# Performance work log

Measured on AMD Instinct MI355X. Metric: run time of the kernel, lower is better.

Reference implementation:

```python
import jax, jax.numpy as jnp
import numpy as np

WS = 7
NHEAD = 8


def setup_inputs() -> dict:
    key = jax.random.key(0)
    k1, k2, k3 = jax.random.split(key, 3)
    B, H, W, D = 32, 56, 56, 256
    x = jax.random.normal(k1, (B, H, W, D), dtype=jnp.float32)
    in_proj_w = jax.random.normal(k2, (3 * D, D), dtype=jnp.float32) * 0.02
    in_proj_b = jnp.zeros((3 * D,), dtype=jnp.float32)
    out_w = jax.random.normal(k3, (D, D), dtype=jnp.float32) * 0.02
    out_b = jnp.zeros((D,), dtype=jnp.float32)
    return {"x": x, "in_proj_w": in_proj_w, "in_proj_b": in_proj_b,
            "out_w": out_w, "out_b": out_b}


def reference(x, in_proj_w, in_proj_b, out_w, out_b):
    B, Hf, Wf, D = x.shape
    ws = WS
    hd = D // NHEAD
    pad_h = (-Hf) % ws
    pad_w = (-Wf) % ws
    xp = jnp.pad(x, ((0, 0), (0, pad_h), (0, pad_w), (0, 0)))
    Hp, Wp = Hf + pad_h, Wf + pad_w
    nh, nw = Hp // ws, Wp // ws
    # partition into windows: [B*nh*nw, ws*ws, D]
    xw = xp.reshape(B, nh, ws, nw, ws, D).transpose(0, 1, 3, 2, 4, 5)
    xw = xw.reshape(B * nh * nw, ws * ws, D)
    N, L = xw.shape[0], ws * ws
    # qkv projection (torch MHA: x @ in_proj_w.T + in_proj_b)
    qkv = jnp.einsum('nld,ed->nle', xw, in_proj_w) + in_proj_b  # [N, L, 3D]
    q, k, v = jnp.split(qkv, 3, axis=-1)
    q = q.reshape(N, L, NHEAD, hd).transpose(0, 2, 1, 3)
    k = k.reshape(N, L, NHEAD, hd).transpose(0, 2, 1, 3)
    v = v.reshape(N, L, NHEAD, hd).transpose(0, 2, 1, 3)
    scale = 1.0 / np.sqrt(hd).astype(np.float32)
    scores = jnp.einsum('nhqd,nhkd->nhqk', q * scale, k)  # [N, H, L, L]
    attn = jax.nn.softmax(scores, axis=-1)
    o = jnp.einsum('nhqk,nhkd->nhqd', attn, v)
    o = o.transpose(0, 2, 1, 3).reshape(N, L, D)
    o = jnp.einsum('nld,ed->nle', o, out_w) + out_b
    # un-window
    o = o.reshape(B, nh, nw, ws, ws, D).transpose(0, 1, 3, 2, 4, 5)
    o = o.reshape(B, Hp, Wp, D)
    return o[:, :Hf, :Wf, :]
```

## Files before the change

### kernel.cpp

```cpp
#include <hip/hip_runtime.h>


using f16   = _Float16;
using f16x4 = __attribute__((ext_vector_type(4))) _Float16;
using f16x8 = __attribute__((ext_vector_type(8))) _Float16;
using f32x4 = __attribute__((ext_vector_type(4))) float;

#define NTOK   100352
#define DMODEL 256
#define QKVN   768

typedef const __attribute__((address_space(1))) unsigned int* as1_u32p;
typedef __attribute__((address_space(3))) unsigned int* as3_u32p;

__device__ __forceinline__ void gload16(const void* g, void* l) {
    __builtin_amdgcn_global_load_lds((as1_u32p)g, (as3_u32p)l, 16, 0, 0);
}

__device__ __forceinline__ f16x8 zero8() {
    f16x8 z;
#pragma unroll
    for (int i = 0; i < 8; ++i) z[i] = (f16)0;
    return z;
}

#define XV4   6422528
#define WQV4  49152
__global__ __launch_bounds__(256) void convert_all(
    const float* __restrict__ X, const float* __restrict__ Wq,
    f16* __restrict__ Xh, f16* __restrict__ Wqh)
{
    const float scale = 0.17677669529663687f;
    const int total = XV4 + WQV4;
    for (int i = blockIdx.x * blockDim.x + threadIdx.x; i < total;
         i += gridDim.x * blockDim.x) {
        float4 f;
        f16x4 h;
        if (i < XV4) {
            f = reinterpret_cast<const float4*>(X)[i];
            h[0]=(f16)f.x; h[1]=(f16)f.y; h[2]=(f16)f.z; h[3]=(f16)f.w;
            reinterpret_cast<f16x4*>(Xh)[i] = h;
        } else {
            int idx = i - XV4;
            int row = idx >> 6;
            float sc = (row < 256) ? scale : 1.0f;
            f = reinterpret_cast<const float4*>(Wq)[idx];
            h[0]=(f16)(f.x*sc); h[1]=(f16)(f.y*sc); h[2]=(f16)(f.z*sc); h[3]=(f16)(f.w*sc);
            reinterpret_cast<f16x4*>(Wqh)[idx] = h;
        }
    }
}

__global__ __launch_bounds__(256) void qkv_gemm(
    const f16* __restrict__ Xh,
    const f16* __restrict__ Wh,
    const float* __restrict__ bias,
    f16* __restrict__ QKV)
{
    __shared__ f16 As[128 * 64];
    __shared__ f16 Bs[128 * 64];
    const int tid  = threadIdx.x;
    const int lane = tid & 63;
    const int wave = tid >> 6;
    int wg = blockIdx.x;
    const int cpx = (NTOK / 128) * (QKVN / 128) / 8;
    wg = (wg & 7) * cpx + (wg >> 3);
    const int m0 = (wg / (QKVN / 128)) * 128;
    const int n0 = (wg % (QKVN / 128)) * 128;
    const int wm = (wave >> 1) * 64;
    const int wn = (wave & 1) * 64;
    const int g  = lane >> 4;
    const int lr = lane & 15;

    f32x4 acc[4][4] = {};

    for (int k0 = 0; k0 < 256; k0 += 64) {
#pragma unroll
        for (int j = 0; j < 4; ++j) {
            int s   = wave * 64 + lane + j * 256;
            int row = s >> 3;
            int cs  = (s & 7) ^ (row & 7);
            gload16(Xh + (size_t)(m0 + row) * 256 + k0 + cs * 8,
                    &As[(size_t)(wave * 64 + j * 256) * 8]);
            gload16(Wh + (size_t)(n0 + row) * 256 + k0 + cs * 8,
                    &Bs[(size_t)(wave * 64 + j * 256) * 8]);
        }
        __syncthreads();
#pragma unroll
        for (int ks = 0; ks < 2; ++ks) {
            f16x8 a[4], b[4];
#pragma unroll
            for (int i = 0; i < 4; ++i) {
                int row = wm + i * 16 + lr;
                int c   = ((ks << 2) + g) ^ (row & 7);
                a[i] = *reinterpret_cast<const f16x8*>(&As[row * 64 + c * 8]);
            }
#pragma unroll
            for (int i = 0; i < 4; ++i) {
                int row = wn + i * 16 + lr;
                int c   = ((ks << 2) + g) ^ (row & 7);
                b[i] = *reinterpret_cast<const f16x8*>(&Bs[row * 64 + c * 8]);
            }
#pragma unroll
            for (int mi = 0; mi < 4; ++mi)
#pragma unroll
                for (int ni = 0; ni < 4; ++ni)
                    acc[mi][ni] = __builtin_amdgcn_mfma_f32_16x16x32_f16(a[mi], b[ni], acc[mi][ni], 0, 0, 0);
        }
        __syncthreads();
    }
    const float scale = 0.17677669529663687f;
#pragma unroll
    for (int ni = 0; ni < 4; ++ni) {
        int n = n0 + wn + ni * 16 + lr;
        float bv = bias[n];
        if (n < 256) bv *= scale;
#pragma unroll
        for (int mi = 0; mi < 4; ++mi)
#pragma unroll
            for (int r = 0; r < 4; ++r) {
                int m = m0 + wm + mi * 16 + g * 4 + r;
                QKV[(size_t)m * QKVN + n] = (f16)(acc[mi][ni][r] + bv);
            }
    }
}

__global__ __launch_bounds__(256) void win_attn(f16* __restrict__ QKV)
{
    __shared__ f16 Vt[4][32][68];
    __shared__ f16 P[4][64][68];
    const int tid  = threadIdx.x;
    const int lane = tid & 63;
    const int w    = tid >> 6;
    const int u    = blockIdx.x * 4 + w;
    const int win = u >> 3, h = u & 7;
    const int b = win >> 6, wh = (win >> 3) & 7, ww = win & 7;
    const int base = (b * 56 + wh * 7) * 56 + ww * 7;
    const int g = lane >> 4, lr = lane & 15;

    auto tok = [&](int row) { int rr = row / 7; return base + rr * 56 + (row - rr * 7); };

    f16x8 qf[4], kf[4];
#pragma unroll
    for (int i = 0; i < 4; ++i) {
        int row = i * 16 + lr;
        if (row < 49) {
            size_t off = (size_t)tok(row) * QKVN + h * 32 + g * 8;
            qf[i] = *reinterpret_cast<const f16x8*>(QKV + off);
            kf[i] = *reinterpret_cast<const f16x8*>(QKV + off + 256);
        } else { qf[i] = zero8(); kf[i] = zero8(); }
    }
    {
        int kk = lane;
        if (kk < 49) {
            size_t off = (size_t)tok(kk) * QKVN + 512 + h * 32;
            f16x8 vv[4];
#pragma unroll
            for (int j = 0; j < 4; ++j)
                vv[j] = *reinterpret_cast<const f16x8*>(QKV + off + j * 8);
#pragma unroll
            for (int j = 0; j < 4; ++j)
#pragma unroll
                for (int d = 0; d < 8; ++d) Vt[w][j * 8 + d][kk] = vv[j][d];
        } else {
#pragma unroll
            for (int d = 0; d < 32; ++d) Vt[w][d][kk] = (f16)0;
        }
    }
    f32x4 s[4][4] = {};
#pragma unroll
    for (int ki = 0; ki < 4; ++ki)
#pragma unroll
        for (int qi = 0; qi < 4; ++qi)
            s[ki][qi] = __builtin_amdgcn_mfma_f32_16x16x32_f16(kf[ki], qf[qi], s[ki][qi], 0, 0, 0);

#pragma unroll
    for (int qi = 0; qi < 4; ++qi) {
        float e[4][4];
        float sum = 0.f;
#pragma unroll
        for (int ki = 0; ki < 4; ++ki)
#pragma unroll
            for (int r = 0; r < 4; ++r)
                e[ki][r] = __expf(s[ki][qi][r]);
#pragma unroll
        for (int ki = 0; ki < 3; ++ki)
#pragma unroll
            for (int r = 0; r < 4; ++r)
                sum += e[ki][r];
        sum += (g == 0) ? e[3][0] : 0.f;
        sum += __shfl_xor(sum, 16, 64);
        sum += __shfl_xor(sum, 32, 64);
        float is = 1.f / sum;
#pragma unroll
        for (int ki = 0; ki < 4; ++ki) {
            f16x4 pw;
            pw[0] = (f16)(e[ki][0] * is);
            pw[1] = (f16)(e[ki][1] * is);
            pw[2] = (f16)(e[ki][2] * is);
            pw[3] = (f16)(e[ki][3] * is);
            *reinterpret_cast<f16x4*>(&P[w][qi * 16 + lr][ki * 16 + g * 4]) = pw;
        }
    }
    __syncthreads();

    f32x4 o[4][2] = {};
#pragma unroll
    for (int ks = 0; ks < 2; ++ks) {
        f16x8 pa[4], vb[2];
#pragma unroll
        for (int mi = 0; mi < 4; ++mi)
            pa[mi] = *reinterpret_cast<const f16x8*>(&P[w][mi * 16 + lr][ks * 32 + g * 8]);
#pragma unroll
        for (int ni = 0; ni < 2; ++ni)
            vb[ni] = *reinterpret_cast<const f16x8*>(&Vt[w][ni * 16 + lr][ks * 32 + g * 8]);
#pragma unroll
        for (int mi = 0; mi < 4; ++mi)
#pragma unroll
            for (int ni = 0; ni < 2; ++ni)
                o[mi][ni] = __builtin_amdgcn_mfma_f32_16x16x32_f16(pa[mi], vb[ni], o[mi][ni], 0, 0, 0);
    }
#pragma unroll
    for (int mi = 0; mi < 4; ++mi)
#pragma unroll
        for (int r = 0; r < 4; ++r) {
            int row = mi * 16 + g * 4 + r;
            if (row < 49) {
                size_t off = (size_t)tok(row) * QKVN + h * 32;
#pragma unroll
                for (int ni = 0; ni < 2; ++ni)
                    QKV[off + ni * 16 + lr] = (f16)o[mi][ni][r];
            }
        }
}

__global__ __launch_bounds__(256) void out_gemm(
    const f16* __restrict__ O,
    const float* __restrict__ W,
    const float* __restrict__ bias,
    float* __restrict__ OUT)
{
    __shared__ f16 As[128 * 64];
    __shared__ f16 Bs[128][72];
    const int tid  = threadIdx.x;
    const int lane = tid & 63;
    const int wave = tid >> 6;
    int wg = blockIdx.x;
    const int cpx = (NTOK / 128) * (DMODEL / 128) / 8;
    wg = (wg & 7) * cpx + (wg >> 3);
    const int m0 = (wg / (DMODEL / 128)) * 128;
    const int n0 = (wg % (DMODEL / 128)) * 128;
    const int wm = (wave >> 1) * 64;
    const int wn = (wave & 1) * 64;
    const int g  = lane >> 4;
    const int lr = lane & 15;

    f32x4 acc[4][4] = {};

    for (int k0 = 0; k0 < 256; k0 += 64) {
#pragma unroll
        for (int j = 0; j < 4; ++j) {
            int s   = wave * 64 + lane + j * 256;
            int row = s >> 3;
            int cs  = (s & 7) ^ (row & 7);
            gload16(O + (size_t)(m0 + row) * QKVN + k0 + cs * 8,
                    &As[(size_t)(wave * 64 + j * 256) * 8]);
        }
#pragma unroll
        for (int j = 0; j < 8; ++j) {
            int v = tid + j * 256;
            int row = v >> 4, cv = v & 15;
            float4 f = *reinterpret_cast<const float4*>(W + (size_t)(n0 + row) * 256 + k0 + cv * 4);
            f16x4 h; h[0]=(f16)f.x; h[1]=(f16)f.y; h[2]=(f16)f.z; h[3]=(f16)f.w;
            *reinterpret_cast<f16x4*>(&Bs[row][cv * 4]) = h;
        }
        __syncthreads();
#pragma unroll
        for (int ks = 0; ks < 2; ++ks) {
            f16x8 a[4], b[4];
#pragma unroll
            for (int i = 0; i < 4; ++i) {
                int row = wm + i * 16 + lr;
                int c   = ((ks << 2) + g) ^ (row & 7);
                a[i] = *reinterpret_cast<const f16x8*>(&As[row * 64 + c * 8]);
            }
#pragma unroll
            for (int i = 0; i < 4; ++i)
                b[i] = *reinterpret_cast<const f16x8*>(&Bs[wn + i * 16 + lr][ks * 32 + g * 8]);
#pragma unroll
            for (int mi = 0; mi < 4; ++mi)
#pragma unroll
                for (int ni = 0; ni < 4; ++ni)
                    acc[mi][ni] = __builtin_amdgcn_mfma_f32_16x16x32_f16(a[mi], b[ni], acc[mi][ni], 0, 0, 0);
        }
        __syncthreads();
    }
#pragma unroll
    for (int ni = 0; ni < 4; ++ni) {
        int n = n0 + wn + ni * 16 + lr;
        float bv = bias[n];
#pragma unroll
        for (int mi = 0; mi < 4; ++mi)
#pragma unroll
            for (int r = 0; r < 4; ++r) {
                int m = m0 + wm + mi * 16 + g * 4 + r;
                OUT[(size_t)m * 256 + n] = acc[mi][ni][r] + bv;
            }
    }
}

extern "C" void kernel_launch(void* const* d_in, const int* in_sizes, int n_in,
                              void* d_out, int out_size, void* d_ws, size_t ws_size,
                              hipStream_t stream) {
    const float* x     = (const float*)d_in[0];
    const float* in_w  = (const float*)d_in[1];
    const float* in_b  = (const float*)d_in[2];
    const float* out_w = (const float*)d_in[3];
    const float* out_b = (const float*)d_in[4];
    float* out = (float*)d_out;
    f16* qkv = (f16*)d_ws;

    f16* xh  = (f16*)d_out;
    f16* wqh = xh + (size_t)NTOK * 256;

    convert_all<<<2048, 256, 0, stream>>>(x, in_w, xh, wqh);

    qkv_gemm<<<(NTOK / 128) * (QKVN / 128), 256, 0, stream>>>(xh, wqh, in_b, qkv);

    win_attn<<<4096, 256, 0, stream>>>(qkv);

    out_gemm<<<(NTOK / 128) * (DMODEL / 128), 256, 0, stream>>>(qkv, out_w, out_b, out);
}
```

Before: 161.3 us.

## Double-buffer A tiles and keep full-K B tile resident in LDS for both GEMMs

Both projection GEMMs now use 512-thread blocks covering 256x128 output tiles. The full K=256 slice of the weight tile is loaded into LDS once up front, and the activation tile is double-buffered so the next K-step's load overlaps the current step's MFMAs. This targets the load-then-sync stalls and halves redundant weight traffic per output row. It raises LDS use to about 128KB per block, which limits occupancy to one block per CU.

```diff
diff --git a/kernel.cpp b/kernel.cpp
--- a/kernel.cpp
+++ b/kernel.cpp
@@ -51,41 +51,57 @@
     }
 }
 
-__global__ __launch_bounds__(256) void qkv_gemm(
+__global__ __launch_bounds__(512) void qkv_gemm(
     const f16* __restrict__ Xh,
     const f16* __restrict__ Wh,
     const float* __restrict__ bias,
     f16* __restrict__ QKV)
 {
-    __shared__ f16 As[128 * 64];
-    __shared__ f16 Bs[128 * 64];
+    __shared__ f16 As[2][256 * 64];
+    __shared__ f16 Bs[128 * 256];
     const int tid  = threadIdx.x;
     const int lane = tid & 63;
     const int wave = tid >> 6;
     int wg = blockIdx.x;
-    const int cpx = (NTOK / 128) * (QKVN / 128) / 8;
+    const int cpx = (NTOK / 256) * (QKVN / 128) / 8;
     wg = (wg & 7) * cpx + (wg >> 3);
-    const int m0 = (wg / (QKVN / 128)) * 128;
+    const int m0 = (wg / (QKVN / 128)) * 256;
     const int n0 = (wg % (QKVN / 128)) * 128;
     const int wm = (wave >> 1) * 64;
     const int wn = (wave & 1) * 64;
     const int g  = lane >> 4;
     const int lr = lane & 15;
 
+#pragma unroll
+    for (int j = 0; j < 8; ++j) {
+        int s   = tid + j * 512;
+        int row = s >> 5, sl = s & 31;
+        int ss  = sl ^ (row & 7);
+        gload16(Wh + (size_t)(n0 + row) * 256 + ss * 8, &Bs[s * 8]);
+    }
+#pragma unroll
+    for (int j = 0; j < 4; ++j) {
+        int s   = tid + j * 512;
+        int row = s >> 3, sl = s & 7;
+        int ss  = sl ^ (row & 7);
+        gload16(Xh + (size_t)(m0 + row) * 256 + ss * 8, &As[0][s * 8]);
+    }
+    __syncthreads();
+
     f32x4 acc[4][4] = {};
-
-    for (int k0 = 0; k0 < 256; k0 += 64) {
-#pragma unroll
-        for (int j = 0; j < 4; ++j) {
-            int s   = wave * 64 + lane + j * 256;
-            int row = s >> 3;
-            int cs  = (s & 7) ^ (row & 7);
-            gload16(Xh + (size_t)(m0 + row) * 256 + k0 + cs * 8,
-                    &As[(size_t)(wave * 64 + j * 256) * 8]);
-            gload16(Wh + (size_t)(n0 + row) * 256 + k0 + cs * 8,
-                    &Bs[(size_t)(wave * 64 + j * 256) * 8]);
-        }
-        __syncthreads();
+    int buf = 0;
+    for (int t = 0; t < 4; ++t) {
+        if (t < 3) {
+            int k0 = (t + 1) * 64;
+#pragma unroll
+            for (int j = 0; j < 4; ++j) {
+                int s   = tid + j * 512;
+                int row = s >> 3, sl = s & 7;
+                int ss  = sl ^ (row & 7);
+                gload16(Xh + (size_t)(m0 + row) * 256 + k0 + ss * 8,
+                        &As[buf ^ 1][s * 8]);
+            }
+        }
 #pragma unroll
         for (int ks = 0; ks < 2; ++ks) {
             f16x8 a[4], b[4];
@@ -93,13 +109,14 @@
             for (int i = 0; i < 4; ++i) {
                 int row = wm + i * 16 + lr;
                 int c   = ((ks << 2) + g) ^ (row & 7);
-                a[i] = *reinterpret_cast<const f16x8*>(&As[row * 64 + c * 8]);
+                a[i] = *reinterpret_cast<const f16x8*>(&As[buf][row * 64 + c * 8]);
             }
 #pragma unroll
             for (int i = 0; i < 4; ++i) {
                 int row = wn + i * 16 + lr;
-                int c   = ((ks << 2) + g) ^ (row & 7);
-                b[i] = *reinterpret_cast<const f16x8*>(&Bs[row * 64 + c * 8]);
+                int sl  = (t << 3) + (ks << 2) + g;
+                int c   = sl ^ (row & 7);
+                b[i] = *reinterpret_cast<const f16x8*>(&Bs[row * 256 + c * 8]);
             }
 #pragma unroll
             for (int mi = 0; mi < 4; ++mi)
@@ -108,6 +125,7 @@
                     acc[mi][ni] = __builtin_amdgcn_mfma_f32_16x16x32_f16(a[mi], b[ni], acc[mi][ni], 0, 0, 0);
         }
         __syncthreads();
+        buf ^= 1;
     }
     const float scale = 0.17677669529663687f;
 #pragma unroll
@@ -234,47 +252,63 @@
         }
 }
 
-__global__ __launch_bounds__(256) void out_gemm(
+__global__ __launch_bounds__(512) void out_gemm(
     const f16* __restrict__ O,
     const float* __restrict__ W,
     const float* __restrict__ bias,
     float* __restrict__ OUT)
 {
-    __shared__ f16 As[128 * 64];
-    __shared__ f16 Bs[128][72];
+    __shared__ f16 As[2][256 * 64];
+    __shared__ f16 Bs[128 * 256];
     const int tid  = threadIdx.x;
     const int lane = tid & 63;
     const int wave = tid >> 6;
     int wg = blockIdx.x;
-    const int cpx = (NTOK / 128) * (DMODEL / 128) / 8;
+    const int cpx = (NTOK / 256) * (DMODEL / 128) / 8;
     wg = (wg & 7) * cpx + (wg >> 3);
-    const int m0 = (wg / (DMODEL / 128)) * 128;
+    const int m0 = (wg / (DMODEL / 128)) * 256;
     const int n0 = (wg % (DMODEL / 128)) * 128;
     const int wm = (wave >> 1) * 64;
     const int wn = (wave & 1) * 64;
     const int g  = lane >> 4;
     const int lr = lane & 15;
 
+#pragma unroll
+    for (int j = 0; j < 8; ++j) {
+        int s   = tid + j * 512;
+        int row = s >> 5, sl = s & 31;
+        const float* wrow = W + (size_t)(n0 + row) * 256 + sl * 8;
+        float4 f0 = *reinterpret_cast<const float4*>(wrow);
+        float4 f1 = *reinterpret_cast<const float4*>(wrow + 4);
+        f16x8 hh;
+        hh[0]=(f16)f0.x; hh[1]=(f16)f0.y; hh[2]=(f16)f0.z; hh[3]=(f16)f0.w;
+        hh[4]=(f16)f1.x; hh[5]=(f16)f1.y; hh[6]=(f16)f1.z; hh[7]=(f16)f1.w;
+        int ss = sl ^ (row & 7);
+        *reinterpret_cast<f16x8*>(&Bs[(row * 32 + ss) * 8]) = hh;
+    }
+#pragma unroll
+    for (int j = 0; j < 4; ++j) {
+        int s   = tid + j * 512;
+        int row = s >> 3, sl = s & 7;
+        int ss  = sl ^ (row & 7);
+        gload16(O + (size_t)(m0 + row) * QKVN + ss * 8, &As[0][s * 8]);
+    }
+    __syncthreads();
+
     f32x4 acc[4][4] = {};
-
-    for (int k0 = 0; k0 < 256; k0 += 64) {
-#pragma unroll
-        for (int j = 0; j < 4; ++j) {
-            int s   = wave * 64 + lane + j * 256;
-            int row = s >> 3;
-            int cs  = (s & 7) ^ (row & 7);
-            gload16(O + (size_t)(m0 + row) * QKVN + k0 + cs * 8,
-                    &As[(size_t)(wave * 64 + j * 256) * 8]);
-        }
-#pragma unroll
-        for (int j = 0; j < 8; ++j) {
-            int v = tid + j * 256;
-            int row = v >> 4, cv = v & 15;
-            float4 f = *reinterpret_cast<const float4*>(W + (size_t)(n0 + row) * 256 + k0 + cv * 4);
-            f16x4 h; h[0]=(f16)f.x; h[1]=(f16)f.y; h[2]=(f16)f.z; h[3]=(f16)f.w;
-            *reinterpret_cast<f16x4*>(&Bs[row][cv * 4]) = h;
-        }
-        __syncthreads();
+    int buf = 0;
+    for (int t = 0; t < 4; ++t) {
+        if (t < 3) {
+            int k0 = (t + 1) * 64;
+#pragma unroll
+            for (int j = 0; j < 4; ++j) {
+                int s   = tid + j * 512;
+                int row = s >> 3, sl = s & 7;
+                int ss  = sl ^ (row & 7);
+                gload16(O + (size_t)(m0 + row) * QKVN + k0 + ss * 8,
+                        &As[buf ^ 1][s * 8]);
+            }
+        }
 #pragma unroll
         for (int ks = 0; ks < 2; ++ks) {
             f16x8 a[4], b[4];
@@ -282,11 +316,15 @@
             for (int i = 0; i < 4; ++i) {
                 int row = wm + i * 16 + lr;
                 int c   = ((ks << 2) + g) ^ (row & 7);
-                a[i] = *reinterpret_cast<const f16x8*>(&As[row * 64 + c * 8]);
-            }
-#pragma unroll
-            for (int i = 0; i < 4; ++i)
-                b[i] = *reinterpret_cast<const f16x8*>(&Bs[wn + i * 16 + lr][ks * 32 + g * 8]);
+                a[i] = *reinterpret_cast<const f16x8*>(&As[buf][row * 64 + c * 8]);
+            }
+#pragma unroll
+            for (int i = 0; i < 4; ++i) {
+                int row = wn + i * 16 + lr;
+                int sl  = (t << 3) + (ks << 2) + g;
+                int c   = sl ^ (row & 7);
+                b[i] = *reinterpret_cast<const f16x8*>(&Bs[row * 256 + c * 8]);
+            }
 #pragma unroll
             for (int mi = 0; mi < 4; ++mi)
 #pragma unroll
@@ -294,6 +332,7 @@
                     acc[mi][ni] = __builtin_amdgcn_mfma_f32_16x16x32_f16(a[mi], b[ni], acc[mi][ni], 0, 0, 0);
         }
         __syncthreads();
+        buf ^= 1;
     }
 #pragma unroll
     for (int ni = 0; ni < 4; ++ni) {
@@ -325,9 +364,9 @@
 
     convert_all<<<2048, 256, 0, stream>>>(x, in_w, xh, wqh);
 
-    qkv_gemm<<<(NTOK / 128) * (QKVN / 128), 256, 0, stream>>>(xh, wqh, in_b, qkv);
+    qkv_gemm<<<(NTOK / 256) * (QKVN / 128), 512, 0, stream>>>(xh, wqh, in_b, qkv);
 
     win_attn<<<4096, 256, 0, stream>>>(qkv);
 
-    out_gemm<<<(NTOK / 128) * (DMODEL / 128), 256, 0, stream>>>(qkv, out_w, out_b, out);
-}
+    out_gemm<<<(NTOK / 256) * (DMODEL / 128), 512, 0, stream>>>(qkv, out_w, out_b, out);
+}
```

New measurement: 177.3 us. 10.0% more time.
